# Kernel tuning notes

Measured on AMD Instinct MI355X. Metric: run time of the kernel, lower is better.

The kernel has to match this reference:

```python
import jax, jax.numpy as jnp
import numpy as np

ROPE_BASE = 10000.0

def apply_rope(x, offset=0):
    # x: [B, H, L, Dh], traditional (interleaved-pair) RoPE
    B, H, L, Dh = x.shape
    pos = jnp.arange(L, dtype=jnp.float32) + offset            # [L]
    freqs = ROPE_BASE ** (-jnp.arange(0, Dh, 2, dtype=jnp.float32) / Dh)  # [Dh/2]
    theta = pos[:, None] * freqs[None, :]                      # [L, Dh/2]
    cos, sin = jnp.cos(theta), jnp.sin(theta)
    x1 = x[..., 0::2]                                          # [B,H,L,Dh/2]
    x2 = x[..., 1::2]
    r1 = x1 * cos - x2 * sin
    r2 = x1 * sin + x2 * cos
    return jnp.stack([r1, r2], axis=-1).reshape(B, H, L, Dh)


def setup_inputs() -> dict:
    key = jax.random.key(0)
    ks = jax.random.split(key, 5)
    B, L, D = 2, 2048, 2048
    s = 1.0 / np.sqrt(D)
    x = jax.random.normal(ks[0], (B, L, D), dtype=jnp.float32)
    # additive causal mask (0 on/below diagonal, -1e9 above)
    mask = jnp.where(jnp.tril(jnp.ones((L, L), dtype=bool)), 0.0, -1e9).astype(jnp.float32)
    Wq = jax.random.normal(ks[1], (D, D), dtype=jnp.float32) * s
    Wk = jax.random.normal(ks[2], (D, D), dtype=jnp.float32) * s
    Wv = jax.random.normal(ks[3], (D, D), dtype=jnp.float32) * s
    Wo = jax.random.normal(ks[4], (D, D), dtype=jnp.float32) * s
    return {"x": x, "mask": mask, "Wq": Wq, "Wk": Wk, "Wv": Wv, "Wo": Wo}


def reference(x, mask, Wq, Wk, Wv, Wo):
    num_heads = 16
    B, L, D = x.shape
    Dh = D // num_heads
    q = (x @ Wq.T).reshape(B, L, num_heads, Dh).transpose(0, 2, 1, 3)  # [B,H,L,Dh]
    k = (x @ Wk.T).reshape(B, L, num_heads, Dh).transpose(0, 2, 1, 3)
    v = (x @ Wv.T).reshape(B, L, num_heads, Dh).transpose(0, 2, 1, 3)
    q = apply_rope(q)
    k = apply_rope(k)
    scale = 1.0 / jnp.sqrt(jnp.float32(Dh))
    scores = jnp.einsum('bhqd,bhkd->bhqk', q * scale, k) + mask  # [B,H,L,L]
    probs = jax.nn.softmax(scores, axis=-1)
    vh = jnp.einsum('bhqk,bhkd->bhqd', probs, v)                 # [B,H,L,Dh]
    vh = vh.transpose(0, 2, 1, 3).reshape(B, L, D)
    out = vh @ Wo.T
    return out, k, v
```

## Files before the change

kernel.cpp:

```cpp
#include <hip/hip_runtime.h>

typedef __attribute__((ext_vector_type(4))) float f32x4;
typedef __attribute__((ext_vector_type(8))) __bf16 bf16x8;

__device__ __forceinline__ unsigned short f2b(float f) {
  unsigned int u = __builtin_bit_cast(unsigned int, f);
  u = (u + 0x7fffu + ((u >> 16) & 1u)) >> 16;
  return (unsigned short)u;
}
__device__ __forceinline__ float b2f(unsigned short h) {
  unsigned int u = ((unsigned int)h) << 16;
  return __builtin_bit_cast(float, u);
}
__device__ __forceinline__ void gl_lds16(const void* g, void* l) {
  __builtin_amdgcn_global_load_lds(
      (const __attribute__((address_space(1))) void*)g,
      (__attribute__((address_space(3))) void*)l, 16, 0, 0);
}

__global__ void cast_kernel(const float* __restrict__ src,
                            unsigned short* __restrict__ dst, int n4) {
  int i = blockIdx.x * blockDim.x + threadIdx.x;
  if (i >= n4) return;
  float4 v = ((const float4*)src)[i];
  ushort4 o;
  o.x = f2b(v.x); o.y = f2b(v.y); o.z = f2b(v.z); o.w = f2b(v.w);
  ((ushort4*)dst)[i] = o;
}

__global__ void cast4_kernel(const float* __restrict__ s0, const float* __restrict__ s1,
                             const float* __restrict__ s2, const float* __restrict__ s3,
                             unsigned short* __restrict__ d0, unsigned short* __restrict__ d1,
                             unsigned short* __restrict__ d2, unsigned short* __restrict__ d3,
                             int n4) {
  int i = blockIdx.x * blockDim.x + threadIdx.x;
  if (i >= n4) return;
  const float* src = blockIdx.y == 0 ? s0 : blockIdx.y == 1 ? s1 : blockIdx.y == 2 ? s2 : s3;
  unsigned short* dst = blockIdx.y == 0 ? d0 : blockIdx.y == 1 ? d1 : blockIdx.y == 2 ? d2 : d3;
  float4 v = ((const float4*)src)[i];
  ushort4 o;
  o.x = f2b(v.x); o.y = f2b(v.y); o.z = f2b(v.z); o.w = f2b(v.w);
  ((ushort4*)dst)[i] = o;
}

__global__ void rope_table_kernel(float2* __restrict__ tab) {
  int idx = blockIdx.x * blockDim.x + threadIdx.x;
  int l = idx >> 6, i = idx & 63;
  float freq = powf(10000.0f, -(float)(2 * i) / 128.0f);
  float th = (float)l * freq;
  tab[idx] = make_float2(cosf(th), sinf(th));
}

__global__ void rope_apply_kernel(unsigned short* __restrict__ qb,
                                  unsigned short* __restrict__ kb,
                                  unsigned short* __restrict__ vb,
                                  float* __restrict__ kout,
                                  float* __restrict__ vout,
                                  const float2* __restrict__ tab) {
  const float QS = 0.12751743f;
  int z = blockIdx.y;
  int p = blockIdx.x * blockDim.x + threadIdx.x;
  int i = p & 63;
  int t = p >> 6;
  int h = t & 15; t >>= 4;
  int l = t & 2047;
  int b = t >> 11;
  int base = ((b * 2048 + l) * 2048) + h * 128 + 2 * i;
  int obase = ((b * 16 + h) * 2048 + l) * 128 + 2 * i;
  if (z == 2) {
    vout[obase] = b2f(vb[base]);
    vout[obase + 1] = b2f(vb[base + 1]);
  } else {
    unsigned short* buf = z ? kb : qb;
    float x1 = b2f(buf[base]), x2 = b2f(buf[base + 1]);
    float2 cs = tab[l * 64 + i];
    float r1 = x1 * cs.x - x2 * cs.y;
    float r2 = x1 * cs.y + x2 * cs.x;
    if (z == 1) {
      buf[base] = f2b(r1);
      buf[base + 1] = f2b(r2);
      kout[obase] = r1; kout[obase + 1] = r2;
    } else {
      buf[base] = f2b(r1 * QS);
      buf[base + 1] = f2b(r2 * QS);
    }
  }
}

__global__ __launch_bounds__(256) void transpose_v_kernel(const unsigned short* __restrict__ vb,
                                                          unsigned short* __restrict__ vt) {
  __shared__ unsigned short t[32][33];
  int bz = blockIdx.z;
  int b = bz >> 4, h = bz & 15;
  int l0 = blockIdx.x * 32, d0 = blockIdx.y * 32;
  const unsigned short* src = vb + (size_t)b * 2048 * 2048 + h * 128;
  unsigned short* dst = vt + (size_t)bz * 128 * 2048;
  int tx = threadIdx.x & 31, ty = threadIdx.x >> 5;
#pragma unroll
  for (int i = 0; i < 4; ++i)
    t[ty + 8 * i][tx] = src[(size_t)(l0 + ty + 8 * i) * 2048 + d0 + tx];
  __syncthreads();
#pragma unroll
  for (int i = 0; i < 4; ++i)
    dst[(size_t)(d0 + ty + 8 * i) * 2048 + l0 + tx] = t[tx][ty + 8 * i];
}

template <int OUT_F32>
__global__ __launch_bounds__(256) void gemm_nt(const unsigned short* __restrict__ A,
                                               const unsigned short* __restrict__ W,
                                               void* __restrict__ C) {
  __shared__ unsigned short As[128 * 32];
  __shared__ unsigned short Bs[128 * 32];
  const int K = 2048, N = 2048;
  int tid = threadIdx.x;
  int lane = tid & 63, wid = tid >> 6;
  int wr = wid >> 1, wc = wid & 1;
  int ln = lane & 15, kg = lane >> 4;
  int m0 = blockIdx.y * 128, n0 = blockIdx.x * 128;

  f32x4 acc[4][4] = {};

  int e0 = tid * 8;
  int r0 = e0 >> 5, c0 = e0 & 31;
  const unsigned short* Ag0 = A + (m0 + r0) * K + c0;
  const unsigned short* Ag1 = A + (m0 + 64 + r0) * K + c0;
  const unsigned short* Wg0 = W + (n0 + r0) * K + c0;
  const unsigned short* Wg1 = W + (n0 + 64 + r0) * K + c0;
  unsigned short* As0 = &As[e0];
  unsigned short* As1 = &As[2048 + e0];
  unsigned short* Bs0 = &Bs[e0];
  unsigned short* Bs1 = &Bs[2048 + e0];

  for (int kt = 0; kt < K; kt += 32) {
    gl_lds16(Ag0 + kt, As0);
    gl_lds16(Ag1 + kt, As1);
    gl_lds16(Wg0 + kt, Bs0);
    gl_lds16(Wg1 + kt, Bs1);
    __syncthreads();
    bf16x8 a[4], bfr[4];
#pragma unroll
    for (int m = 0; m < 4; ++m)
      a[m] = *(const bf16x8*)&As[(wr * 64 + m * 16 + ln) * 32 + kg * 8];
#pragma unroll
    for (int n = 0; n < 4; ++n)
      bfr[n] = *(const bf16x8*)&Bs[(wc * 64 + n * 16 + ln) * 32 + kg * 8];
#pragma unroll
    for (int m = 0; m < 4; ++m)
#pragma unroll
      for (int n = 0; n < 4; ++n)
        acc[m][n] = __builtin_amdgcn_mfma_f32_16x16x32_bf16(a[m], bfr[n], acc[m][n], 0, 0, 0);
    __syncthreads();
  }

  int row0 = m0 + wr * 64, col0 = n0 + wc * 64;
#pragma unroll
  for (int m = 0; m < 4; ++m)
#pragma unroll
    for (int n = 0; n < 4; ++n)
#pragma unroll
      for (int j = 0; j < 4; ++j) {
        int r = row0 + m * 16 + kg * 4 + j;
        int c = col0 + n * 16 + ln;
        float v = acc[m][n][j];
        if (OUT_F32)
          ((float*)C)[r * N + c] = v;
        else
          ((unsigned short*)C)[r * N + c] = f2b(v);
      }
}

__global__ __launch_bounds__(256, 2) void attn3_kernel(const unsigned short* __restrict__ Qb,
                                                       const unsigned short* __restrict__ Kb,
                                                       const unsigned short* __restrict__ Vt,
                                                       unsigned short* __restrict__ Ob) {
  __shared__ unsigned short KS[2][8192];
  __shared__ unsigned short VS[2][8192];
  __shared__ unsigned short PS[4][2048];
  const int D = 2048, L = 2048;
  int tid = threadIdx.x, lane = tid & 63, w = tid >> 6;
  int ln = lane & 15, kg = lane >> 4;
  int bid = blockIdx.x;
  int g = bid >> 5, bh = bid & 31;
  int qt = (g < 8) ? (15 - g) : (g - 8);
  int b = bh >> 4, h = bh & 15;
  const size_t base = (size_t)b * L * D + h * 128;
  const unsigned short* Kp = Kb + base;
  const unsigned short* Qp = Qb + base;
  unsigned short* Op = Ob + base;
  const unsigned short* Vp = Vt + (size_t)bh * 128 * L;

  int q0 = qt * 128;
  int qw0 = q0 + w * 32;

  bf16x8 aq[2][4];
#pragma unroll
  for (int m = 0; m < 2; ++m)
#pragma unroll
    for (int kc = 0; kc < 4; ++kc)
      aq[m][kc] = *(const bf16x8*)&Qp[(size_t)(qw0 + m * 16 + ln) * D + kc * 32 + kg * 8];

  f32x4 o[2][8] = {};
  float m2[2][4], ls[2][4];
#pragma unroll
  for (int m = 0; m < 2; ++m)
#pragma unroll
    for (int j = 0; j < 4; ++j) { m2[m][j] = -1e30f; ls[m][j] = 0.f; }

  int l16 = lane >> 4, l8 = lane >> 3, l7 = lane & 7;

#define STAGE(T, NB)                                                                   \
  {                                                                                    \
    int kv0_ = (T) << 6;                                                               \
    _Pragma("unroll") for (int i = 0; i < 4; ++i) {                                    \
      int cK = w * 4 + i;                                                              \
      int r = cK * 4 + l16;                                                            \
      int sw = ln ^ (r & 7);                                                           \
      gl_lds16(Kp + (size_t)(kv0_ + r) * D + sw * 8, &KS[NB][cK * 512 + lane * 8]);    \
      int dh = cK * 8 + l8;                                                            \
      int sv = l7 ^ (dh & 7);                                                          \
      gl_lds16(Vp + (size_t)dh * L + kv0_ + sv * 8, &VS[NB][cK * 512 + lane * 8]);     \
    }                                                                                  \
  }

  int nt = 2 * qt + 2;
  int mask_t = 2 * qt + (w >> 1);

  STAGE(0, 0);
  __syncthreads();

  for (int t = 0; t < nt; ++t) {
    int cur = t & 1;
    if (t + 1 < nt) STAGE(t + 1, cur ^ 1);

    if (t <= mask_t) {
      int kv0 = t << 6;
      f32x4 s[2][4] = {};
#pragma unroll
      for (int n = 0; n < 4; ++n)
#pragma unroll
        for (int kc = 0; kc < 4; ++kc) {
          bf16x8 bk = *(const bf16x8*)&KS[cur][(n * 16 + ln) * 128 + (((kc << 2) + kg) ^ (ln & 7)) * 8];
          s[0][n] = __builtin_amdgcn_mfma_f32_16x16x32_bf16(aq[0][kc], bk, s[0][n], 0, 0, 0);
          s[1][n] = __builtin_amdgcn_mfma_f32_16x16x32_bf16(aq[1][kc], bk, s[1][n], 0, 0, 0);
        }
      if (t == mask_t) {
#pragma unroll
        for (int m = 0; m < 2; ++m)
#pragma unroll
          for (int n = 0; n < 4; ++n)
#pragma unroll
            for (int j = 0; j < 4; ++j)
              if (kv0 + n * 16 + ln > qw0 + m * 16 + kg * 4 + j) s[m][n][j] = -1e30f;
      }
      float pmax[2][4];
      bool near = true;
#pragma unroll
      for (int m = 0; m < 2; ++m)
#pragma unroll
        for (int j = 0; j < 4; ++j) {
          pmax[m][j] = fmaxf(fmaxf(s[m][0][j], s[m][1][j]), fmaxf(s[m][2][j], s[m][3][j]));
          near = near && (pmax[m][j] <= m2[m][j] + 8.0f);
        }
      if (!__all(near)) {
#pragma unroll
        for (int m = 0; m < 2; ++m)
#pragma unroll
          for (int j = 0; j < 4; ++j) {
            float mx = pmax[m][j];
#pragma unroll
            for (int d = 1; d < 16; d <<= 1) mx = fmaxf(mx, __shfl_xor(mx, d));
            mx = fmaxf(mx, m2[m][j]);
            float al = __builtin_amdgcn_exp2f(m2[m][j] - mx);
            m2[m][j] = mx;
            ls[m][j] *= al;
#pragma unroll
            for (int dt = 0; dt < 8; ++dt) o[m][dt][j] *= al;
          }
      }
#pragma unroll
      for (int m = 0; m < 2; ++m)
#pragma unroll
        for (int j = 0; j < 4; ++j) {
          int row = m * 16 + kg * 4 + j;
          float acc = 0.f;
#pragma unroll
          for (int n = 0; n < 4; ++n) {
            float p = __builtin_amdgcn_exp2f(s[m][n][j] - m2[m][j]);
            acc += p;
            unsigned int u = __builtin_bit_cast(unsigned int, p);
            PS[w][row * 64 + (((n * 2 + (ln >> 3)) ^ (row & 7)) * 8) + (ln & 7)] =
                (unsigned short)(u >> 16);
          }
          ls[m][j] += acc;
        }
#pragma unroll
      for (int kst = 0; kst < 2; ++kst) {
        bf16x8 ap0 = *(const bf16x8*)&PS[w][(ln) * 64 + (((kst << 2) + kg) ^ (ln & 7)) * 8];
        bf16x8 ap1 = *(const bf16x8*)&PS[w][(16 + ln) * 64 + (((kst << 2) + kg) ^ (ln & 7)) * 8];
#pragma unroll
        for (int dt = 0; dt < 8; ++dt) {
          bf16x8 bv = *(const bf16x8*)&VS[cur][(dt * 16 + ln) * 64 + (((kst << 2) + kg) ^ (ln & 7)) * 8];
          o[0][dt] = __builtin_amdgcn_mfma_f32_16x16x32_bf16(ap0, bv, o[0][dt], 0, 0, 0);
          o[1][dt] = __builtin_amdgcn_mfma_f32_16x16x32_bf16(ap1, bv, o[1][dt], 0, 0, 0);
        }
      }
    }
    __syncthreads();
  }
#undef STAGE

#pragma unroll
  for (int m = 0; m < 2; ++m)
#pragma unroll
    for (int j = 0; j < 4; ++j) {
      float tsum = ls[m][j];
#pragma unroll
      for (int d = 1; d < 16; d <<= 1) tsum += __shfl_xor(tsum, d);
      float inv = 1.0f / tsum;
      int row = qw0 + m * 16 + kg * 4 + j;
#pragma unroll
      for (int dt = 0; dt < 8; ++dt)
        Op[(size_t)row * D + dt * 16 + ln] = f2b(o[m][dt][j] * inv);
    }
}

extern "C" void kernel_launch(void* const* d_in, const int* in_sizes, int n_in,
                              void* d_out, int out_size, void* d_ws, size_t ws_size,
                              hipStream_t stream) {
  const float* x  = (const float*)d_in[0];
  const float* Wq = (const float*)d_in[2];
  const float* Wk = (const float*)d_in[3];
  const float* Wv = (const float*)d_in[4];
  const float* Wo = (const float*)d_in[5];

  char* ws = (char*)d_ws;
  unsigned short* xb  = (unsigned short*)(ws + 0);
  unsigned short* wqb = (unsigned short*)(ws + 16777216);
  unsigned short* wkb = (unsigned short*)(ws + 25165824);
  unsigned short* wvb = (unsigned short*)(ws + 33554432);
  unsigned short* wob = (unsigned short*)(ws + 41943040);
  unsigned short* qb  = (unsigned short*)(ws + 50331648);
  unsigned short* kb  = (unsigned short*)(ws + 67108864);
  unsigned short* vb  = (unsigned short*)(ws + 83886080);
  float2* tab         = (float2*)(ws + 100663296);
  unsigned short* vt  = wqb;
  unsigned short* ob  = xb;

  float* out  = (float*)d_out;
  float* kout = out + 8388608;
  float* vout = out + 16777216;

  cast_kernel<<<8192, 256, 0, stream>>>(x, xb, 2097152);
  cast4_kernel<<<dim3(4096, 4), 256, 0, stream>>>(Wq, Wk, Wv, Wo, wqb, wkb, wvb, wob, 1048576);
  rope_table_kernel<<<512, 256, 0, stream>>>(tab);

  dim3 gg(16, 32);
  gemm_nt<0><<<gg, 256, 0, stream>>>(xb, wqb, qb);
  gemm_nt<0><<<gg, 256, 0, stream>>>(xb, wkb, kb);
  gemm_nt<0><<<gg, 256, 0, stream>>>(xb, wvb, vb);

  transpose_v_kernel<<<dim3(64, 4, 32), 256, 0, stream>>>(vb, vt);

  rope_apply_kernel<<<dim3(16384, 3), 256, 0, stream>>>(qb, kb, vb, kout, vout, tab);

  attn3_kernel<<<512, 256, 0, stream>>>(qb, kb, vt, ob);

  gemm_nt<1><<<gg, 256, 0, stream>>>(ob, wob, out);
}
```

Baseline: 331.0 us.

## Fuse QKV projections into one double-buffered 128x256 GEMM with swizzled LDS

Replaces the single-buffered 128x128 GEMM with a 512-thread kernel that computes 128x256 tiles and a K-step of 64. It double-buffers global-to-LDS loads interleaved with the MFMA work, XOR-swizzles LDS to avoid bank conflicts, and remaps block order for L2 locality. The three Q/K/V projections become one launch, relying on the contiguous layout of wqb/wkb/wvb and of qb/kb/vb. Costs are higher LDS and register use per block and reliance on that buffer adjacency.

```diff
diff --git a/kernel.cpp b/kernel.cpp
--- a/kernel.cpp
+++ b/kernel.cpp
@@ -105,68 +105,121 @@
     dst[(size_t)(d0 + ty + 8 * i) * 2048 + l0 + tx] = t[tx][ty + 8 * i];
 }
 
-template <int OUT_F32>
-__global__ __launch_bounds__(256) void gemm_nt(const unsigned short* __restrict__ A,
-                                               const unsigned short* __restrict__ W,
-                                               void* __restrict__ C) {
-  __shared__ unsigned short As[128 * 32];
-  __shared__ unsigned short Bs[128 * 32];
-  const int K = 2048, N = 2048;
-  int tid = threadIdx.x;
-  int lane = tid & 63, wid = tid >> 6;
-  int wr = wid >> 1, wc = wid & 1;
+template <int NBN, int OUT_F32>
+__global__ __launch_bounds__(512, 2) void gemm2(const unsigned short* __restrict__ A,
+                                                const unsigned short* __restrict__ W,
+                                                void* __restrict__ C) {
+  __shared__ unsigned short As[2][128 * 64];
+  __shared__ unsigned short Bs[2][256 * 64];
+  const int K = 2048, NT = 32;
+  int tid = threadIdx.x, lane = tid & 63, w = tid >> 6;
+  int wr = w >> 2, wc = w & 3;
   int ln = lane & 15, kg = lane >> 4;
-  int m0 = blockIdx.y * 128, n0 = blockIdx.x * 128;
+
+  int cpx = gridDim.x >> 3;
+  int swz = (blockIdx.x & 7) * cpx + (blockIdx.x >> 3);
+  int bm = swz / NBN, bn = swz % NBN;
+  int m0 = bm * 128, n0 = bn * 256;
+
+  int trow = tid >> 3;
+  int sg = ((tid & 7) ^ (trow & 7)) * 8;
+  const unsigned short* pA0 = A + (size_t)(m0 + trow) * K + sg;
+  const unsigned short* pA1 = pA0 + (size_t)64 * K;
+  const unsigned short* pB0 = W + (size_t)(n0 + trow) * K + sg;
+  const unsigned short* pB1 = pB0 + (size_t)64 * K;
+  const unsigned short* pB2 = pB0 + (size_t)128 * K;
+  const unsigned short* pB3 = pB0 + (size_t)192 * K;
+
+  int sw0 = (kg ^ (ln & 7)) * 8;
+  int sw1 = ((4 + kg) ^ (ln & 7)) * 8;
+  int arow = wr * 64 + ln;
+  int brow = wc * 64 + ln;
 
   f32x4 acc[4][4] = {};
 
-  int e0 = tid * 8;
-  int r0 = e0 >> 5, c0 = e0 & 31;
-  const unsigned short* Ag0 = A + (m0 + r0) * K + c0;
-  const unsigned short* Ag1 = A + (m0 + 64 + r0) * K + c0;
-  const unsigned short* Wg0 = W + (n0 + r0) * K + c0;
-  const unsigned short* Wg1 = W + (n0 + 64 + r0) * K + c0;
-  unsigned short* As0 = &As[e0];
-  unsigned short* As1 = &As[2048 + e0];
-  unsigned short* Bs0 = &Bs[e0];
-  unsigned short* Bs1 = &Bs[2048 + e0];
-
-  for (int kt = 0; kt < K; kt += 32) {
-    gl_lds16(Ag0 + kt, As0);
-    gl_lds16(Ag1 + kt, As1);
-    gl_lds16(Wg0 + kt, Bs0);
-    gl_lds16(Wg1 + kt, Bs1);
-    __syncthreads();
-    bf16x8 a[4], bfr[4];
-#pragma unroll
-    for (int m = 0; m < 4; ++m)
-      a[m] = *(const bf16x8*)&As[(wr * 64 + m * 16 + ln) * 32 + kg * 8];
-#pragma unroll
-    for (int n = 0; n < 4; ++n)
-      bfr[n] = *(const bf16x8*)&Bs[(wc * 64 + n * 16 + ln) * 32 + kg * 8];
-#pragma unroll
-    for (int m = 0; m < 4; ++m)
-#pragma unroll
-      for (int n = 0; n < 4; ++n)
-        acc[m][n] = __builtin_amdgcn_mfma_f32_16x16x32_bf16(a[m], bfr[n], acc[m][n], 0, 0, 0);
+  gl_lds16(pA0, &As[0][tid * 8]);
+  gl_lds16(pA1, &As[0][4096 + tid * 8]);
+  gl_lds16(pB0, &Bs[0][tid * 8]);
+  gl_lds16(pB1, &Bs[0][4096 + tid * 8]);
+  gl_lds16(pB2, &Bs[0][8192 + tid * 8]);
+  gl_lds16(pB3, &Bs[0][12288 + tid * 8]);
+  __syncthreads();
+
+  for (int t = 0; t < NT; ++t) {
+    int cur = t & 1, nb = cur ^ 1;
+    int ko = (t + 1) * 64;
+    bool more = (t + 1) < NT;
+    const unsigned short* Ac = As[cur];
+    const unsigned short* Bc = Bs[cur];
+    bf16x8 a[4], b0, b1;
+
+#pragma unroll
+    for (int m = 0; m < 4; ++m) a[m] = *(const bf16x8*)&Ac[(arow + m * 16) * 64 + sw0];
+    b0 = *(const bf16x8*)&Bc[(brow + 0) * 64 + sw0];
+    b1 = *(const bf16x8*)&Bc[(brow + 16) * 64 + sw0];
+    if (more) { gl_lds16(pA0 + ko, &As[nb][tid * 8]); gl_lds16(pB0 + ko, &Bs[nb][tid * 8]); }
+    __builtin_amdgcn_s_setprio(1);
+#pragma unroll
+    for (int m = 0; m < 4; ++m) {
+      acc[m][0] = __builtin_amdgcn_mfma_f32_16x16x32_bf16(a[m], b0, acc[m][0], 0, 0, 0);
+      acc[m][1] = __builtin_amdgcn_mfma_f32_16x16x32_bf16(a[m], b1, acc[m][1], 0, 0, 0);
+    }
+    __builtin_amdgcn_s_setprio(0);
+
+    b0 = *(const bf16x8*)&Bc[(brow + 32) * 64 + sw0];
+    b1 = *(const bf16x8*)&Bc[(brow + 48) * 64 + sw0];
+    if (more) { gl_lds16(pA1 + ko, &As[nb][4096 + tid * 8]); gl_lds16(pB1 + ko, &Bs[nb][4096 + tid * 8]); }
+    __builtin_amdgcn_s_setprio(1);
+#pragma unroll
+    for (int m = 0; m < 4; ++m) {
+      acc[m][2] = __builtin_amdgcn_mfma_f32_16x16x32_bf16(a[m], b0, acc[m][2], 0, 0, 0);
+      acc[m][3] = __builtin_amdgcn_mfma_f32_16x16x32_bf16(a[m], b1, acc[m][3], 0, 0, 0);
+    }
+    __builtin_amdgcn_s_setprio(0);
+
+#pragma unroll
+    for (int m = 0; m < 4; ++m) a[m] = *(const bf16x8*)&Ac[(arow + m * 16) * 64 + sw1];
+    b0 = *(const bf16x8*)&Bc[(brow + 0) * 64 + sw1];
+    b1 = *(const bf16x8*)&Bc[(brow + 16) * 64 + sw1];
+    if (more) gl_lds16(pB2 + ko, &Bs[nb][8192 + tid * 8]);
+    __builtin_amdgcn_s_setprio(1);
+#pragma unroll
+    for (int m = 0; m < 4; ++m) {
+      acc[m][0] = __builtin_amdgcn_mfma_f32_16x16x32_bf16(a[m], b0, acc[m][0], 0, 0, 0);
+      acc[m][1] = __builtin_amdgcn_mfma_f32_16x16x32_bf16(a[m], b1, acc[m][1], 0, 0, 0);
+    }
+    __builtin_amdgcn_s_setprio(0);
+
+    b0 = *(const bf16x8*)&Bc[(brow + 32) * 64 + sw1];
+    b1 = *(const bf16x8*)&Bc[(brow + 48) * 64 + sw1];
+    if (more) gl_lds16(pB3 + ko, &Bs[nb][12288 + tid * 8]);
+    __builtin_amdgcn_s_setprio(1);
+#pragma unroll
+    for (int m = 0; m < 4; ++m) {
+      acc[m][2] = __builtin_amdgcn_mfma_f32_16x16x32_bf16(a[m], b0, acc[m][2], 0, 0, 0);
+      acc[m][3] = __builtin_amdgcn_mfma_f32_16x16x32_bf16(a[m], b1, acc[m][3], 0, 0, 0);
+    }
+    __builtin_amdgcn_s_setprio(0);
+
     __syncthreads();
   }
 
-  int row0 = m0 + wr * 64, col0 = n0 + wc * 64;
+  int mat = bn >> 3;
+  size_t cbase = (size_t)mat * 8388608 + (size_t)((bn & 7) * 256 + wc * 64 + ln);
 #pragma unroll
   for (int m = 0; m < 4; ++m)
 #pragma unroll
-    for (int n = 0; n < 4; ++n)
-#pragma unroll
-      for (int j = 0; j < 4; ++j) {
-        int r = row0 + m * 16 + kg * 4 + j;
-        int c = col0 + n * 16 + ln;
+    for (int j = 0; j < 4; ++j) {
+      size_t r = (size_t)(m0 + wr * 64 + m * 16 + kg * 4 + j) * 2048 + cbase;
+#pragma unroll
+      for (int n = 0; n < 4; ++n) {
         float v = acc[m][n][j];
         if (OUT_F32)
-          ((float*)C)[r * N + c] = v;
+          ((float*)C)[r + n * 16] = v;
         else
-          ((unsigned short*)C)[r * N + c] = f2b(v);
+          ((unsigned short*)C)[r + n * 16] = f2b(v);
       }
+    }
 }
 
 __global__ __launch_bounds__(256, 2) void attn3_kernel(const unsigned short* __restrict__ Qb,
@@ -354,10 +407,7 @@
   cast4_kernel<<<dim3(4096, 4), 256, 0, stream>>>(Wq, Wk, Wv, Wo, wqb, wkb, wvb, wob, 1048576);
   rope_table_kernel<<<512, 256, 0, stream>>>(tab);
 
-  dim3 gg(16, 32);
-  gemm_nt<0><<<gg, 256, 0, stream>>>(xb, wqb, qb);
-  gemm_nt<0><<<gg, 256, 0, stream>>>(xb, wkb, kb);
-  gemm_nt<0><<<gg, 256, 0, stream>>>(xb, wvb, vb);
+  gemm2<24, 0><<<768, 512, 0, stream>>>(xb, wqb, qb);
 
   transpose_v_kernel<<<dim3(64, 4, 32), 256, 0, stream>>>(vb, vt);
 
@@ -365,5 +415,5 @@
 
   attn3_kernel<<<512, 256, 0, stream>>>(qb, kb, vt, ob);
 
-  gemm_nt<1><<<gg, 256, 0, stream>>>(ob, wob, out);
-}
+  gemm2<8, 1><<<256, 512, 0, stream>>>(ob, wob, out);
+}
```

Measured after the change: 354.3 us. +7.0%, slower.

## Replace GEMMs with double-buffered 256-wide tiled kernel and fuse QKV projections

Applied to the files above, without the earlier changes.

Replaces the simple single-buffered 128x128 bf16 GEMM with a 512-thread kernel using 256-wide N tiles, XOR-swizzled LDS, double-buffered async global-to-LDS loads with explicit vmcnt waits and barriers, and an XCD-aware block swizzle. The three Q/K/V projections become one launch that treats the contiguous Wq/Wk/Wv buffers as a single 6144-row weight and writes each third to the matching contiguous qb/kb/vb output. The aim is to overlap memory with MFMA work, cut LDS bank conflicts and launch count. In exchange it relies on the workspace layout being contiguous and on hand-tuned wait counts, which is fragile.

```diff
diff --git a/kernel.cpp b/kernel.cpp
--- a/kernel.cpp
+++ b/kernel.cpp
@@ -105,68 +105,128 @@
     dst[(size_t)(d0 + ty + 8 * i) * 2048 + l0 + tx] = t[tx][ty + 8 * i];
 }
 
-template <int OUT_F32>
-__global__ __launch_bounds__(256) void gemm_nt(const unsigned short* __restrict__ A,
-                                               const unsigned short* __restrict__ W,
-                                               void* __restrict__ C) {
-  __shared__ unsigned short As[128 * 32];
-  __shared__ unsigned short Bs[128 * 32];
-  const int K = 2048, N = 2048;
-  int tid = threadIdx.x;
-  int lane = tid & 63, wid = tid >> 6;
-  int wr = wid >> 1, wc = wid & 1;
-  int ln = lane & 15, kg = lane >> 4;
-  int m0 = blockIdx.y * 128, n0 = blockIdx.x * 128;
-
-  f32x4 acc[4][4] = {};
-
-  int e0 = tid * 8;
-  int r0 = e0 >> 5, c0 = e0 & 31;
-  const unsigned short* Ag0 = A + (m0 + r0) * K + c0;
-  const unsigned short* Ag1 = A + (m0 + 64 + r0) * K + c0;
-  const unsigned short* Wg0 = W + (n0 + r0) * K + c0;
-  const unsigned short* Wg1 = W + (n0 + 64 + r0) * K + c0;
-  unsigned short* As0 = &As[e0];
-  unsigned short* As1 = &As[2048 + e0];
-  unsigned short* Bs0 = &Bs[e0];
-  unsigned short* Bs1 = &Bs[2048 + e0];
-
-  for (int kt = 0; kt < K; kt += 32) {
-    gl_lds16(Ag0 + kt, As0);
-    gl_lds16(Ag1 + kt, As1);
-    gl_lds16(Wg0 + kt, Bs0);
-    gl_lds16(Wg1 + kt, Bs1);
-    __syncthreads();
-    bf16x8 a[4], bfr[4];
-#pragma unroll
-    for (int m = 0; m < 4; ++m)
-      a[m] = *(const bf16x8*)&As[(wr * 64 + m * 16 + ln) * 32 + kg * 8];
-#pragma unroll
-    for (int n = 0; n < 4; ++n)
-      bfr[n] = *(const bf16x8*)&Bs[(wc * 64 + n * 16 + ln) * 32 + kg * 8];
-#pragma unroll
-    for (int m = 0; m < 4; ++m)
-#pragma unroll
-      for (int n = 0; n < 4; ++n)
-        acc[m][n] = __builtin_amdgcn_mfma_f32_16x16x32_bf16(a[m], bfr[n], acc[m][n], 0, 0, 0);
-    __syncthreads();
+template <int BM, int NBN, int OUT_F32>
+__global__ __launch_bounds__(512, 2) void gemm3(const unsigned short* __restrict__ A,
+                                                const unsigned short* __restrict__ W,
+                                                void* __restrict__ C) {
+  constexpr int K = 2048, NT = 32;
+  constexpr int AH = BM / 2;
+  constexpr int MF = BM / 64;
+  constexpr int AQ = AH / 64;
+  __shared__ unsigned short Asm[2][2][AH * 64];
+  __shared__ unsigned short Bsm[2][2][128 * 64];
+
+  const int tid = threadIdx.x, lane = tid & 63, wv = tid >> 6;
+  const int wr = wv >> 2, wc = wv & 3;
+  const int ln = lane & 15, kg = lane >> 4;
+
+  const int cpx = (int)gridDim.x >> 3;
+  const int swzb = ((int)blockIdx.x & 7) * cpx + ((int)blockIdx.x >> 3);
+  const int bm = swzb / NBN, bn = swzb % NBN;
+  const int m0 = bm * BM, n0 = bn * 256;
+
+  const int rr = lane >> 3;
+  const int sws = ((lane & 7) ^ (rr & 7)) * 8;
+  const unsigned short* pA = A + (size_t)(m0 + wv * 8 * AQ + rr) * K + sws;
+  const unsigned short* pB = W + (size_t)(n0 + wv * 16 + rr) * K + sws;
+
+#define STA_(dd, hh, tt)                                                         \
+  _Pragma("unroll") for (int q = 0; q < AQ; ++q)                                 \
+      gl_lds16(pA + ((size_t)(hh)*AH + q * 8) * K + (size_t)(tt)*64,             \
+               &Asm[dd][hh][(wv * 8 * AQ + q * 8) * 64 + lane * 8]);
+#define STB_(dd, hh, tt)                                                         \
+  _Pragma("unroll") for (int q = 0; q < 2; ++q)                                  \
+      gl_lds16(pB + ((size_t)(hh)*128 + q * 8) * K + (size_t)(tt)*64,            \
+               &Bsm[dd][hh][(wv * 16 + q * 8) * 64 + lane * 8]);
+
+  const int sw0 = (kg ^ (ln & 7)) * 8;
+  const int sw1 = ((4 + kg) ^ (ln & 7)) * 8;
+  const int rae = (wr * (AH / 2) + ln) * 64;
+  const int rbe = (wc * 32 + ln) * 64;
+
+  f32x4 acc[2 * MF][4] = {};
+  bf16x8 aA[MF][2], bB[2][2];
+
+#define QUAD(dd, mh, bh, LA, LB)                                                  \
+  {                                                                               \
+    if (LA) {                                                                     \
+      _Pragma("unroll") for (int mf = 0; mf < MF; ++mf) {                         \
+        aA[mf][0] = *(const bf16x8*)&Asm[dd][mh][rae + mf * 1024 + sw0];          \
+        aA[mf][1] = *(const bf16x8*)&Asm[dd][mh][rae + mf * 1024 + sw1];          \
+      }                                                                           \
+    }                                                                             \
+    if (LB) {                                                                     \
+      _Pragma("unroll") for (int nf = 0; nf < 2; ++nf) {                          \
+        bB[nf][0] = *(const bf16x8*)&Bsm[dd][bh][rbe + nf * 1024 + sw0];          \
+        bB[nf][1] = *(const bf16x8*)&Bsm[dd][bh][rbe + nf * 1024 + sw1];          \
+      }                                                                           \
+    }                                                                             \
+    __builtin_amdgcn_s_setprio(1);                                                \
+    _Pragma("unroll") for (int mf = 0; mf < MF; ++mf)                             \
+        _Pragma("unroll") for (int nf = 0; nf < 2; ++nf) {                        \
+      acc[(mh)*MF + mf][(bh)*2 + nf] = __builtin_amdgcn_mfma_f32_16x16x32_bf16(   \
+          aA[mf][0], bB[nf][0], acc[(mh)*MF + mf][(bh)*2 + nf], 0, 0, 0);         \
+      acc[(mh)*MF + mf][(bh)*2 + nf] = __builtin_amdgcn_mfma_f32_16x16x32_bf16(   \
+          aA[mf][1], bB[nf][1], acc[(mh)*MF + mf][(bh)*2 + nf], 0, 0, 0);         \
+    }                                                                             \
+    __builtin_amdgcn_s_setprio(0);                                                \
   }
 
-  int row0 = m0 + wr * 64, col0 = n0 + wc * 64;
-#pragma unroll
-  for (int m = 0; m < 4; ++m)
-#pragma unroll
-    for (int n = 0; n < 4; ++n)
+#define BAR                                                                       \
+  __builtin_amdgcn_s_barrier();                                                   \
+  __builtin_amdgcn_sched_barrier(0);
+#define VWAIT                                                                     \
+  if (BM == 256) { asm volatile("s_waitcnt vmcnt(4)" ::: "memory"); }             \
+  else { asm volatile("s_waitcnt vmcnt(3)" ::: "memory"); }
+
+  STA_(0, 0, 0); STB_(0, 0, 0); STB_(0, 1, 0); STA_(0, 1, 0);
+  STA_(1, 0, 1); STB_(1, 1, 1);
+  VWAIT; BAR;
+
+  for (int T = 0; T < NT; T += 2) {
+    const bool more = (T + 2) < NT;
+    STB_(1, 0, T + 1);            QUAD(0, 0, 0, 1, 1); BAR;
+    STA_(1, 1, T + 1);            QUAD(0, 0, 1, 0, 1); BAR;
+    if (more) STA_(0, 0, T + 2);  QUAD(0, 1, 1, 1, 0); BAR;
+    if (more) STB_(0, 1, T + 2);  QUAD(0, 1, 0, 0, 1);
+    if (more) { VWAIT; } else { asm volatile("s_waitcnt vmcnt(0)" ::: "memory"); }
+    BAR;
+    if (more) STB_(0, 0, T + 2);  QUAD(1, 0, 0, 1, 1); BAR;
+    if (more) STA_(0, 1, T + 2);  QUAD(1, 0, 1, 0, 1); BAR;
+    if (more) STA_(1, 0, T + 3);  QUAD(1, 1, 1, 1, 0); BAR;
+    if (more) {
+      STB_(1, 1, T + 3);          QUAD(1, 1, 0, 0, 1); VWAIT; BAR;
+    } else {
+      QUAD(1, 1, 0, 0, 1);
+    }
+  }
+
+  const int mat = bn >> 3;
+  unsigned short* Cb = (unsigned short*)C;
+  float* Cf = (float*)C;
+#pragma unroll
+  for (int mh = 0; mh < 2; ++mh)
+#pragma unroll
+    for (int mf = 0; mf < MF; ++mf)
 #pragma unroll
       for (int j = 0; j < 4; ++j) {
-        int r = row0 + m * 16 + kg * 4 + j;
-        int c = col0 + n * 16 + ln;
-        float v = acc[m][n][j];
-        if (OUT_F32)
-          ((float*)C)[r * N + c] = v;
-        else
-          ((unsigned short*)C)[r * N + c] = f2b(v);
+        int row = m0 + mh * AH + wr * (AH / 2) + mf * 16 + kg * 4 + j;
+        size_t rb = (size_t)mat * 8388608 + (size_t)row * 2048 + (size_t)((bn & 7) * 256);
+#pragma unroll
+        for (int bh = 0; bh < 2; ++bh)
+#pragma unroll
+          for (int nf = 0; nf < 2; ++nf) {
+            int col = bh * 128 + wc * 32 + nf * 16 + ln;
+            float v = acc[mh * MF + mf][bh * 2 + nf][j];
+            if (OUT_F32) Cf[rb + col] = v;
+            else Cb[rb + col] = f2b(v);
+          }
       }
+#undef STA_
+#undef STB_
+#undef QUAD
+#undef BAR
+#undef VWAIT
 }
 
 __global__ __launch_bounds__(256, 2) void attn3_kernel(const unsigned short* __restrict__ Qb,
@@ -354,10 +414,7 @@
   cast4_kernel<<<dim3(4096, 4), 256, 0, stream>>>(Wq, Wk, Wv, Wo, wqb, wkb, wvb, wob, 1048576);
   rope_table_kernel<<<512, 256, 0, stream>>>(tab);
 
-  dim3 gg(16, 32);
-  gemm_nt<0><<<gg, 256, 0, stream>>>(xb, wqb, qb);
-  gemm_nt<0><<<gg, 256, 0, stream>>>(xb, wkb, kb);
-  gemm_nt<0><<<gg, 256, 0, stream>>>(xb, wvb, vb);
+  gemm3<256, 24, 0><<<384, 512, 0, stream>>>(xb, wqb, qb);
 
   transpose_v_kernel<<<dim3(64, 4, 32), 256, 0, stream>>>(vb, vt);
 
@@ -365,5 +422,5 @@
 
   attn3_kernel<<<512, 256, 0, stream>>>(qb, kb, vt, ob);
 
-  gemm_nt<1><<<gg, 256, 0, stream>>>(ob, wob, out);
-}
+  gemm3<128, 8, 1><<<256, 512, 0, stream>>>(ob, wob, out);
+}
```

Measured after the change: 327.9 us. About the same (-0.9%).
